# Optimization experiments

Measured on AMD Instinct MI355X. Metric: run time of the kernel, lower is better.

## Reference

```python
import jax, jax.numpy as jnp
import numpy as np

B, C_IN, C_OUT, N = 16, 256, 256, 1024


def setup_inputs() -> dict:
    key = jax.random.key(0)
    k1, k2, k3, k4, k5 = jax.random.split(key, 5)
    x = jax.random.normal(k1, (B, C_IN, N), dtype=jnp.float32)
    adj1 = jax.random.uniform(k2, (B, N, N), dtype=jnp.float32)
    adj2 = jax.random.uniform(k3, (B, N, N), dtype=jnp.float32)
    # weight init: normal(0, 0.01) as in reset_parameters
    weight = jax.random.normal(k4, (C_OUT, C_IN), dtype=jnp.float32) * 0.01
    stdv = 1.0 / np.sqrt(C_IN)
    bias = jax.random.uniform(k5, (1, C_OUT, 1), minval=-stdv, maxval=stdv, dtype=jnp.float32)
    return {"x": x, "adj1": adj1, "adj2": adj2, "weight": weight, "bias": bias}


def reference(x, adj1, adj2, weight, bias):
    half = weight.shape[0] // 2
    # per-sample chained matmul: W_half @ (x_i @ A_i), batched
    xa1 = jnp.einsum('bcn,bnm->bcm', x, adj1)          # [B, C_in, N]
    xa2 = jnp.einsum('bcn,bnm->bcm', x, adj2)          # [B, C_in, N]
    out1 = jnp.einsum('oc,bcm->bom', weight[:half], xa1)  # [B, C_out/2, N]
    out2 = jnp.einsum('oc,bcm->bom', weight[half:], xa2)  # [B, C_out/2, N]
    out = jnp.concatenate([out1, out2], axis=1) + bias     # [B, C_out, N]
    return jax.nn.relu(out)
```

## Files before the change

kernel.cpp:

```cpp
#include <hip/hip_runtime.h>
#include <hip/hip_bf16.h>

typedef unsigned short u16;
typedef unsigned int u32;
typedef __attribute__((ext_vector_type(8))) short bf16x8;
typedef __attribute__((ext_vector_type(4))) float f32x4;

__device__ __forceinline__ u16 f2bf(float f) {
  return __builtin_bit_cast(u16, __float2bfloat16(f));
}

__device__ __forceinline__ bf16x8 ld_frag16(const u16* p) {
  return __builtin_bit_cast(bf16x8, *reinterpret_cast<const uint4*>(p));
}

__device__ __forceinline__ void gload_lds16(const void* g, void* l) {
  __builtin_amdgcn_global_load_lds((const __attribute__((address_space(1))) void*)g,
                                   (__attribute__((address_space(3))) void*)l, 16, 0, 0);
}

__global__ __launch_bounds__(256, 3) void gemm1(
    const float* __restrict__ x, const float* __restrict__ weight,
    u16* __restrict__ Y)
{
  constexpr int Nn = 1024, K = 256, BK = 32, SB = 40;
  __shared__ __align__(16) u16 As[128 * 32];
  __shared__ __align__(16) u16 Bs[64 * SB];

  const int t = threadIdx.x;
  const int b = blockIdx.z, mt = blockIdx.y, n0 = blockIdx.x * 64;

  const float* Wp = weight + (size_t)mt * 128 * K;
  const float* Xb = x + (size_t)b * K * Nn;

  const int w = t >> 6, l = t & 63;
  const int wm = w >> 1, wn = w & 1;
  const int lr = l & 15, lg = l >> 4;

  const int ar = t >> 1, akc = (t & 1) * 16;
  const int bm = t & 63, bkq = t >> 6;
  const float* Xcol = Xb + n0 + bm;

  f32x4 acc[4][2] = {};

  for (int kt = 0; kt < K / BK; ++kt) {
    const int k0 = kt * BK;

    float4 a4[4];
#pragma unroll
    for (int uu = 0; uu < 4; ++uu)
      a4[uu] = reinterpret_cast<const float4*>(Wp + (size_t)ar * K + k0 + akc)[uu];
    union { uint4 q[2]; u16 s[16]; } ua;
#pragma unroll
    for (int uu = 0; uu < 4; ++uu) {
      ua.s[uu * 4 + 0] = f2bf(a4[uu].x); ua.s[uu * 4 + 1] = f2bf(a4[uu].y);
      ua.s[uu * 4 + 2] = f2bf(a4[uu].z); ua.s[uu * 4 + 3] = f2bf(a4[uu].w);
    }
    {
      const int c0 = akc >> 3;
      const int sw = (ar >> 1) & 3;
      uint4* Aq = reinterpret_cast<uint4*>(As);
      Aq[ar * 4 + ((c0 + 0) ^ sw)] = ua.q[0];
      Aq[ar * 4 + ((c0 + 1) ^ sw)] = ua.q[1];
    }

    float v[8];
#pragma unroll
    for (int j = 0; j < 8; ++j)
      v[j] = Xcol[(size_t)(k0 + bkq * 8 + j) * Nn];
    union { uint4 q; u16 s[8]; } ub;
#pragma unroll
    for (int j = 0; j < 8; ++j) ub.s[j] = f2bf(v[j]);
    reinterpret_cast<uint4*>(Bs)[bm * 5 + bkq] = ub.q;

    __syncthreads();

    bf16x8 af[4], bfr[2];
#pragma unroll
    for (int mi = 0; mi < 4; ++mi) {
      const int rr = wm * 64 + mi * 16 + lr;
      const int cw = lg ^ ((rr >> 1) & 3);
      af[mi] = ld_frag16(As + rr * BK + cw * 8);
    }
#pragma unroll
    for (int ni = 0; ni < 2; ++ni) {
      const int cc = wn * 32 + ni * 16 + lr;
      bfr[ni] = ld_frag16(Bs + cc * SB + lg * 8);
    }
#pragma unroll
    for (int mi = 0; mi < 4; ++mi)
#pragma unroll
      for (int ni = 0; ni < 2; ++ni)
        acc[mi][ni] = __builtin_amdgcn_mfma_f32_16x16x32_bf16(
            af[mi], bfr[ni], acc[mi][ni], 0, 0, 0);

    __syncthreads();
  }

#pragma unroll
  for (int mi = 0; mi < 4; ++mi) {
#pragma unroll
    for (int rr = 0; rr < 4; ++rr) {
      const int row = mt * 128 + wm * 64 + mi * 16 + lg * 4 + rr;
      u16* Yrow = Y + ((size_t)(b * 256 + row)) * Nn + n0;
#pragma unroll
      for (int ni = 0; ni < 2; ++ni) {
        const int col = wn * 32 + ni * 16 + lr;
        Yrow[col] = f2bf(acc[mi][ni][rr]);
      }
    }
  }
}

__global__ __launch_bounds__(256, 3) void gemm2(
    const float* __restrict__ adj1, const float* __restrict__ adj2,
    const u16* __restrict__ Y, const float* __restrict__ bias,
    float* __restrict__ out)
{
  constexpr int Nn = 1024, BK = 32, SB = 40;
  __shared__ __align__(16) u16 As[128 * 32];
  __shared__ __align__(16) u16 Bs[64 * SB];

  const int t = threadIdx.x;
  const int b = blockIdx.z, h = blockIdx.y, n0 = blockIdx.x * 64;

  const float* adj = (h == 0 ? adj1 : adj2) + (size_t)b * Nn * Nn;
  const u16* Yb = Y + ((size_t)(b * 256 + h * 128)) * Nn;

  const int w = t >> 6, l = t & 63;
  const int wm = w >> 1, wn = w & 1;
  const int lr = l & 15, lg = l >> 4;

  const int bm = t & 63, bkq = t >> 6;
  const float* adjcol = adj + n0 + bm;

  f32x4 acc[4][2] = {};

  for (int kt = 0; kt < Nn / BK; ++kt) {
    const int k0 = kt * BK;

#pragma unroll
    for (int j = 0; j < 2; ++j) {
      const int chunkbase = j * 256 + w * 64;
      const int chunk = chunkbase + l;
      const int r = chunk >> 2, c = chunk & 3;
      const int cg = c ^ ((r >> 1) & 3);
      gload_lds16(Yb + (size_t)r * Nn + k0 + cg * 8,
                  (void*)(As + chunkbase * 8));
    }

    float v[8];
#pragma unroll
    for (int j = 0; j < 8; ++j)
      v[j] = adjcol[(size_t)(k0 + bkq * 8 + j) * Nn];
    union { uint4 q; u16 s[8]; } ub;
#pragma unroll
    for (int j = 0; j < 8; ++j) ub.s[j] = f2bf(v[j]);
    reinterpret_cast<uint4*>(Bs)[bm * 5 + bkq] = ub.q;

    __syncthreads();

    bf16x8 af[4], bfr[2];
#pragma unroll
    for (int mi = 0; mi < 4; ++mi) {
      const int rr = wm * 64 + mi * 16 + lr;
      const int cw = lg ^ ((rr >> 1) & 3);
      af[mi] = ld_frag16(As + rr * BK + cw * 8);
    }
#pragma unroll
    for (int ni = 0; ni < 2; ++ni) {
      const int cc = wn * 32 + ni * 16 + lr;
      bfr[ni] = ld_frag16(Bs + cc * SB + lg * 8);
    }
#pragma unroll
    for (int mi = 0; mi < 4; ++mi)
#pragma unroll
      for (int ni = 0; ni < 2; ++ni)
        acc[mi][ni] = __builtin_amdgcn_mfma_f32_16x16x32_bf16(
            af[mi], bfr[ni], acc[mi][ni], 0, 0, 0);

    __syncthreads();
  }

#pragma unroll
  for (int mi = 0; mi < 4; ++mi) {
#pragma unroll
    for (int rr = 0; rr < 4; ++rr) {
      const int go = h * 128 + wm * 64 + mi * 16 + lg * 4 + rr;
      const float bi = bias[go];
      float* orow = out + ((size_t)(b * 256 + go)) * Nn + n0;
#pragma unroll
      for (int ni = 0; ni < 2; ++ni) {
        const int col = wn * 32 + ni * 16 + lr;
        orow[col] = fmaxf(acc[mi][ni][rr] + bi, 0.f);
      }
    }
  }
}

extern "C" void kernel_launch(void* const* d_in, const int* in_sizes, int n_in,
                              void* d_out, int out_size, void* d_ws, size_t ws_size,
                              hipStream_t stream) {
  const float* x    = (const float*)d_in[0];
  const float* adj1 = (const float*)d_in[1];
  const float* adj2 = (const float*)d_in[2];
  const float* wgt  = (const float*)d_in[3];
  const float* bias = (const float*)d_in[4];
  float* out = (float*)d_out;
  u16* Y = (u16*)d_ws;

  dim3 blk(256);
  dim3 g1(16, 2, 16);
  gemm1<<<g1, blk, 0, stream>>>(x, wgt, Y);
  dim3 g2(16, 2, 16);
  gemm2<<<g2, blk, 0, stream>>>(adj1, adj2, Y, bias, out);
}
```

Baseline: 52.65 us.

## Double-buffer gemm2 LDS tiles and use 512-thread blocks with smaller per-wave tiles

Gemm2 now keeps two LDS buffers and prefetches the next K-tile of Y (global_load_lds) and adj while MFMAs run on the current tile, so there is a single barrier per iteration. The block grows to 8 waves, each owning a 32x32 sub-tile, and each thread loads 4 adj values instead of 8. The goal is to hide global load latency on the bandwidth-heavy adj stream. In exchange, LDS use doubles and per-wave work shrinks, which may affect occupancy.

```diff
diff --git a/kernel.cpp b/kernel.cpp
--- a/kernel.cpp
+++ b/kernel.cpp
@@ -112,14 +112,14 @@
   }
 }
 
-__global__ __launch_bounds__(256, 3) void gemm2(
+__global__ __launch_bounds__(512, 4) void gemm2(
     const float* __restrict__ adj1, const float* __restrict__ adj2,
     const u16* __restrict__ Y, const float* __restrict__ bias,
     float* __restrict__ out)
 {
-  constexpr int Nn = 1024, BK = 32, SB = 40;
-  __shared__ __align__(16) u16 As[128 * 32];
-  __shared__ __align__(16) u16 Bs[64 * SB];
+  constexpr int Nn = 1024, BK = 32, SB = 40, NT = Nn / BK;
+  __shared__ __align__(16) u16 As[2][128 * 32];
+  __shared__ __align__(16) u16 Bs[2][64 * SB];
 
   const int t = threadIdx.x;
   const int b = blockIdx.z, h = blockIdx.y, n0 = blockIdx.x * 64;
@@ -131,62 +131,93 @@
   const int wm = w >> 1, wn = w & 1;
   const int lr = l & 15, lg = l >> 4;
 
-  const int bm = t & 63, bkq = t >> 6;
+  const int a_r = t >> 2, a_c = t & 3;
+  const int a_cg = a_c ^ ((a_r >> 1) & 3);
+  const u16* a_src = Yb + (size_t)a_r * Nn + a_cg * 8;
+  const int a_dstoff = (w * 64) * 8;
+
+  const int bm = l, bkq = w;
   const float* adjcol = adj + n0 + bm;
-
-  f32x4 acc[4][2] = {};
-
-  for (int kt = 0; kt < Nn / BK; ++kt) {
-    const int k0 = kt * BK;
-
-#pragma unroll
-    for (int j = 0; j < 2; ++j) {
-      const int chunkbase = j * 256 + w * 64;
-      const int chunk = chunkbase + l;
-      const int r = chunk >> 2, c = chunk & 3;
-      const int cg = c ^ ((r >> 1) & 3);
-      gload_lds16(Yb + (size_t)r * Nn + k0 + cg * 8,
-                  (void*)(As + chunkbase * 8));
-    }
-
-    float v[8];
-#pragma unroll
-    for (int j = 0; j < 8; ++j)
-      v[j] = adjcol[(size_t)(k0 + bkq * 8 + j) * Nn];
-    union { uint4 q; u16 s[8]; } ub;
-#pragma unroll
-    for (int j = 0; j < 8; ++j) ub.s[j] = f2bf(v[j]);
-    reinterpret_cast<uint4*>(Bs)[bm * 5 + bkq] = ub.q;
-
-    __syncthreads();
-
-    bf16x8 af[4], bfr[2];
-#pragma unroll
-    for (int mi = 0; mi < 4; ++mi) {
-      const int rr = wm * 64 + mi * 16 + lr;
+  const int b_dstoff = bm * SB + bkq * 4;
+
+  f32x4 acc[2][2] = {};
+
+  gload_lds16(a_src, (void*)(&As[0][0] + a_dstoff));
+  {
+    float v[4];
+#pragma unroll
+    for (int j = 0; j < 4; ++j) v[j] = adjcol[(size_t)(bkq * 4 + j) * Nn];
+    union { uint2 q; u16 s[4]; } ub;
+#pragma unroll
+    for (int j = 0; j < 4; ++j) ub.s[j] = f2bf(v[j]);
+    *reinterpret_cast<uint2*>(&Bs[0][0] + b_dstoff) = ub.q;
+  }
+  __syncthreads();
+
+  int cur = 0;
+  for (int kt = 0; kt < NT - 1; ++kt) {
+    const int k1 = (kt + 1) * BK;
+    const int nxt = cur ^ 1;
+
+    gload_lds16(a_src + k1, (void*)(&As[nxt][0] + a_dstoff));
+    float v[4];
+#pragma unroll
+    for (int j = 0; j < 4; ++j) v[j] = adjcol[(size_t)(k1 + bkq * 4 + j) * Nn];
+
+    bf16x8 af[2], bfr[2];
+#pragma unroll
+    for (int mi = 0; mi < 2; ++mi) {
+      const int rr = wm * 32 + mi * 16 + lr;
       const int cw = lg ^ ((rr >> 1) & 3);
-      af[mi] = ld_frag16(As + rr * BK + cw * 8);
+      af[mi] = ld_frag16(&As[cur][0] + rr * BK + cw * 8);
     }
 #pragma unroll
     for (int ni = 0; ni < 2; ++ni) {
       const int cc = wn * 32 + ni * 16 + lr;
-      bfr[ni] = ld_frag16(Bs + cc * SB + lg * 8);
-    }
-#pragma unroll
-    for (int mi = 0; mi < 4; ++mi)
+      bfr[ni] = ld_frag16(&Bs[cur][0] + cc * SB + lg * 8);
+    }
+#pragma unroll
+    for (int mi = 0; mi < 2; ++mi)
 #pragma unroll
       for (int ni = 0; ni < 2; ++ni)
         acc[mi][ni] = __builtin_amdgcn_mfma_f32_16x16x32_bf16(
             af[mi], bfr[ni], acc[mi][ni], 0, 0, 0);
 
+    union { uint2 q; u16 s[4]; } ub;
+#pragma unroll
+    for (int j = 0; j < 4; ++j) ub.s[j] = f2bf(v[j]);
+    *reinterpret_cast<uint2*>(&Bs[nxt][0] + b_dstoff) = ub.q;
+
     __syncthreads();
-  }
-
-#pragma unroll
-  for (int mi = 0; mi < 4; ++mi) {
+    cur = nxt;
+  }
+
+  {
+    bf16x8 af[2], bfr[2];
+#pragma unroll
+    for (int mi = 0; mi < 2; ++mi) {
+      const int rr = wm * 32 + mi * 16 + lr;
+      const int cw = lg ^ ((rr >> 1) & 3);
+      af[mi] = ld_frag16(&As[cur][0] + rr * BK + cw * 8);
+    }
+#pragma unroll
+    for (int ni = 0; ni < 2; ++ni) {
+      const int cc = wn * 32 + ni * 16 + lr;
+      bfr[ni] = ld_frag16(&Bs[cur][0] + cc * SB + lg * 8);
+    }
+#pragma unroll
+    for (int mi = 0; mi < 2; ++mi)
+#pragma unroll
+      for (int ni = 0; ni < 2; ++ni)
+        acc[mi][ni] = __builtin_amdgcn_mfma_f32_16x16x32_bf16(
+            af[mi], bfr[ni], acc[mi][ni], 0, 0, 0);
+  }
+
+#pragma unroll
+  for (int mi = 0; mi < 2; ++mi) {
 #pragma unroll
     for (int rr = 0; rr < 4; ++rr) {
-      const int go = h * 128 + wm * 64 + mi * 16 + lg * 4 + rr;
+      const int go = h * 128 + wm * 32 + mi * 16 + lg * 4 + rr;
       const float bi = bias[go];
       float* orow = out + ((size_t)(b * 256 + go)) * Nn + n0;
 #pragma unroll
@@ -209,9 +240,8 @@
   float* out = (float*)d_out;
   u16* Y = (u16*)d_ws;
 
-  dim3 blk(256);
   dim3 g1(16, 2, 16);
-  gemm1<<<g1, blk, 0, stream>>>(x, wgt, Y);
+  gemm1<<<g1, dim3(256), 0, stream>>>(x, wgt, Y);
   dim3 g2(16, 2, 16);
-  gemm2<<<g2, blk, 0, stream>>>(adj1, adj2, Y, bias, out);
-}
+  gemm2<<<g2, dim3(512), 0, stream>>>(adj1, adj2, Y, bias, out);
+}
```

New measurement: 57.27 us. 8.8% more time.
